# Kernel optimization log

Measured on AMD Instinct MI355X. Metric: run time of the kernel, lower is better.

## Reference

```python
import jax, jax.numpy as jnp
import numpy as np

THRESHOLD = 6.2
N_SECTIONS = 9      # n_conv_sections
SEC_LEN = 4         # n_section_length
SEC_H = 9           # n_input_sections + n_section_length - 1
BATCH = 16384


def setup_inputs() -> dict:
    key = jax.random.key(0)
    k1, k2 = jax.random.split(key)
    # input spike-wave tensor [T, C=1, H=41, W=40]
    x = jax.random.uniform(k1, (BATCH, 1, 41, 40), dtype=jnp.float32)
    # per-section conv weights, N(0.8, 0.05) as in snn.Convolution init
    W = 0.8 + 0.05 * jax.random.normal(k2, (N_SECTIONS, 50, 1, 6, 40), dtype=jnp.float32)
    return {"x": x, "W": W}


def _conv(sec, w):
    # sec: [B,1,9,40], w: [50,1,6,40] -> [B,50,4,1]
    return jax.lax.conv_general_dilated(
        sec, w, window_strides=(1, 1), padding='VALID',
        dimension_numbers=('NCHW', 'OIHW', 'NCHW'))


def reference(x, W):
    # slice the 9 overlapping input sections -> [9, B, 1, 9, 40]
    sec = jnp.stack([x[:, :, i * SEC_LEN:i * SEC_LEN + SEC_H, :]
                     for i in range(N_SECTIONS)])
    pots = jax.vmap(_conv)(sec, W)                      # [9, B, 50, 4, 1]
    pots = jnp.max(pots, axis=3, keepdims=True)         # Pooling((4,1)) -> [9, B, 50, 1, 1]
    spks = jnp.where(pots > THRESHOLD, 1.0, 0.0).astype(pots.dtype)
    # concat sections along height (dim=2 of [B,C,H,W])
    pots_cat = jnp.moveaxis(pots[:, :, :, 0, :], 0, 2)  # [B, 50, 9, 1]
    spks_cat = jnp.moveaxis(spks[:, :, :, 0, :], 0, 2)  # [B, 50, 9, 1]
    return pots_cat, spks_cat
```

## Files before the change

### kernel.cpp

```cpp
#include <hip/hip_runtime.h>
#include <cstdint>
#include <cstddef>

#define NBATCH   16384
#define NSEC     9
#define NOC      50
#define NOCP     64
#define KPAD     256
#define KREAL    240
#define XROW     1640
#define XUNITS   208
#define XSF      1664
#define TB       16
#define OUTHALF  7372800
#define THRESH   6.2f

typedef _Float16 half8  __attribute__((ext_vector_type(8)));
typedef float    f32x4  __attribute__((ext_vector_type(4)));

__global__ __launch_bounds__(256)
void wconv_kernel(const float* __restrict__ W, _Float16* __restrict__ wks) {
    int idx = blockIdx.x * 256 + threadIdx.x;
    int k   = idx & 255;
    int ocp = (idx >> 8) & 63;
    int sec = idx >> 14;
    float v = 0.0f;
    if (ocp < NOC && k < KREAL)
        v = W[(size_t)(sec * NOC + ocp) * KREAL + k];
    wks[idx] = (_Float16)v;
}

__global__ __launch_bounds__(256, 3)
void fused_kernel(const float* __restrict__ x,
                  const _Float16* __restrict__ wks,
                  float* __restrict__ out) {
    __shared__ __align__(16) _Float16 xs[TB * XSF];

    const int tid = threadIdx.x;
    const size_t b0 = (size_t)blockIdx.x * TB;

    {
        const int bb  = tid >> 4;
        const int u16 = tid & 15;
        const int sw  = bb & 7;
        const float* xrow = x + (b0 + bb) * XROW;
        _Float16* lrow = xs + bb * XSF;

        #pragma unroll
        for (int c = 0; c < 2; ++c) {
            const int jn = c ? 6 : 7;
            float4 va[7], vb[7];
            #pragma unroll
            for (int jj = 0; jj < 7; ++jj) {
                if (jj < jn) {
                    int u = u16 + 16 * (c * 7 + jj);
                    if (u < 205) {
                        va[jj] = *(const float4*)(xrow + u * 8);
                        vb[jj] = *(const float4*)(xrow + u * 8 + 4);
                    } else {
                        va[jj] = float4{0, 0, 0, 0};
                        vb[jj] = float4{0, 0, 0, 0};
                    }
                }
            }
            #pragma unroll
            for (int jj = 0; jj < 7; ++jj) {
                if (jj < jn) {
                    int u = u16 + 16 * (c * 7 + jj);
                    half8 h;
                    h[0] = (_Float16)va[jj].x; h[1] = (_Float16)va[jj].y;
                    h[2] = (_Float16)va[jj].z; h[3] = (_Float16)va[jj].w;
                    h[4] = (_Float16)vb[jj].x; h[5] = (_Float16)vb[jj].y;
                    h[6] = (_Float16)vb[jj].z; h[7] = (_Float16)vb[jj].w;
                    *(half8*)(lrow + ((u ^ sw) << 3)) = h;
                }
            }
        }
    }
    __syncthreads();

    const int lane = tid & 63;
    const int w    = tid >> 6;
    const int l15  = lane & 15;
    const int quad = lane >> 4;
    const int sw   = l15 & 7;

    const _Float16* arow = xs + l15 * XSF;
    const _Float16* wrow = wks + (size_t)(w * 16 + l15) * KPAD + quad * 8;

    f32x4 res[NSEC];

    for (int s = 0; s < NSEC; ++s) {
        const _Float16* wsec = wrow + (size_t)s * (NOCP * KPAD);
        half8 bv[8];
        #pragma unroll
        for (int kk = 0; kk < 8; ++kk)
            bv[kk] = *(const half8*)(wsec + kk * 32);

        f32x4 acc[4] = {f32x4{}, f32x4{}, f32x4{}, f32x4{}};
        const int su = s * 20 + quad;
        #pragma unroll
        for (int kk = 0; kk < 8; ++kk) {
            #pragma unroll
            for (int h = 0; h < 4; ++h) {
                int unit = su + h * 5 + kk * 4;
                half8 av = *(const half8*)(arow + ((unit ^ sw) << 3));
                acc[h] = __builtin_amdgcn_mfma_f32_16x16x32_f16(
                             av, bv[kk], acc[h], 0, 0, 0);
            }
        }
        f32x4 r;
        #pragma unroll
        for (int j = 0; j < 4; ++j)
            r[j] = fmaxf(fmaxf(acc[0][j], acc[1][j]),
                         fmaxf(acc[2][j], acc[3][j]));
        res[s] = r;
    }

    __syncthreads();
    float* t = (float*)xs;
    const int oc = w * 16 + l15;
    if (oc < NOC) {
        #pragma unroll
        for (int s = 0; s < NSEC; ++s)
            #pragma unroll
            for (int r = 0; r < 4; ++r)
                t[(quad * 4 + r) * 450 + oc * 9 + s] = res[s][r];
    }
    __syncthreads();

    const size_t ob = b0 * 450;
    for (int i = tid; i < TB * 450; i += 256) {
        float v = t[i];
        out[ob + i] = v;
        out[OUTHALF + ob + i] = (v > THRESH) ? 1.0f : 0.0f;
    }
}

__global__ __launch_bounds__(256)
void naive_kernel(const float* __restrict__ x, const float* __restrict__ W,
                  float* __restrict__ out) {
    size_t idx = (size_t)blockIdx.x * 256 + threadIdx.x;
    if (idx >= OUTHALF) return;
    int s  = (int)(idx % NSEC);
    int oc = (int)((idx / NSEC) % NOC);
    int b  = (int)(idx / (NSEC * NOC));
    const float* xb = x + (size_t)b * XROW + s * 160;
    const float* wv = W + (size_t)(s * NOC + oc) * KREAL;
    float best = -1e30f;
    for (int h0 = 0; h0 < 4; ++h0) {
        float acc = 0.0f;
        for (int k = 0; k < KREAL; ++k)
            acc += xb[h0 * 40 + k] * wv[k];
        best = fmaxf(best, acc);
    }
    out[idx] = best;
    out[OUTHALF + idx] = (best > THRESH) ? 1.0f : 0.0f;
}

extern "C" void kernel_launch(void* const* d_in, const int* in_sizes, int n_in,
                              void* d_out, int out_size, void* d_ws, size_t ws_size,
                              hipStream_t stream) {
    const float* x = (const float*)d_in[0];
    const float* W = (const float*)d_in[1];
    float* out = (float*)d_out;

    const size_t w_bytes = (size_t)NSEC * NOCP * KPAD * sizeof(_Float16);

    if (ws_size < w_bytes) {
        naive_kernel<<<(OUTHALF + 255) / 256, 256, 0, stream>>>(x, W, out);
        return;
    }

    _Float16* wks = (_Float16*)d_ws;

    wconv_kernel<<<(NSEC * NOCP * KPAD) / 256, 256, 0, stream>>>(W, wks);
    fused_kernel<<<NBATCH / TB, 256, 0, stream>>>(x, wks, out);
}
```

Baseline: 216.1 us.

## Pre-convert input to swizzled fp16 and DMA it into LDS, split sections across waves

A prep kernel now converts x to fp16 in a pre-swizzled tile layout alongside the weight conversion. The main kernel loads each tile straight into LDS with global_load_lds. Each wave now owns a subset of sections and computes all 64 output channels, reusing A fragments across four B tiles. This adds a full extra read/write pass over x in fp16 through workspace, and pooled potentials are rounded to fp16 before storing, which can flip threshold decisions near 6.2.

Measured after the change: 244.2 us. 13.0% more time.

```diff
diff --git a/kernel.cpp b/kernel.cpp
--- a/kernel.cpp
+++ b/kernel.cpp
@@ -12,95 +12,200 @@
 #define XUNITS   208
 #define XSF      1664
 #define TB       16
+#define NTILES   1024
+#define TILEF16  26624
+#define WELEMS   147456
+#define WBLOCKS  576
 #define OUTHALF  7372800
 #define THRESH   6.2f
 
 typedef _Float16 half8  __attribute__((ext_vector_type(8)));
+typedef _Float16 half4v __attribute__((ext_vector_type(4)));
 typedef float    f32x4  __attribute__((ext_vector_type(4)));
 
+#define GLD_LDS16(gsrc, ldst)                                                  \
+    __builtin_amdgcn_global_load_lds(                                          \
+        (const __attribute__((address_space(1))) void*)(gsrc),                 \
+        (__attribute__((address_space(3))) void*)(ldst), 16, 0, 0)
+
 __global__ __launch_bounds__(256)
-void wconv_kernel(const float* __restrict__ W, _Float16* __restrict__ wks) {
-    int idx = blockIdx.x * 256 + threadIdx.x;
-    int k   = idx & 255;
-    int ocp = (idx >> 8) & 63;
-    int sec = idx >> 14;
-    float v = 0.0f;
-    if (ocp < NOC && k < KREAL)
-        v = W[(size_t)(sec * NOC + ocp) * KREAL + k];
-    wks[idx] = (_Float16)v;
+void prep_kernel(const float* __restrict__ x, const float* __restrict__ W,
+                 _Float16* __restrict__ wks, _Float16* __restrict__ x16) {
+    const int blk = blockIdx.x, tid = threadIdx.x;
+    if (blk < WBLOCKS) {
+        int idx = blk * 256 + tid;
+        int k   = idx & 255;
+        int ocp = (idx >> 8) & 63;
+        int sec = idx >> 14;
+        float v = 0.0f;
+        if (ocp < NOC && k < KREAL)
+            v = W[(size_t)(sec * NOC + ocp) * KREAL + k];
+        wks[idx] = (_Float16)v;
+        return;
+    }
+    const int b2   = blk - WBLOCKS;
+    const int tile = b2 / 13;
+    const int rem  = (b2 - tile * 13) * 256 + tid;
+    const int brow = rem / XUNITS;
+    const int slot = rem - brow * XUNITS;
+    const int u    = slot ^ (brow & 7);
+    half8 h = {};
+    if (u < 205) {
+        const float* src = x + ((size_t)tile * TB + brow) * XROW + u * 8;
+        float4 a = *(const float4*)src;
+        float4 b = *(const float4*)(src + 4);
+        h[0] = (_Float16)a.x; h[1] = (_Float16)a.y;
+        h[2] = (_Float16)a.z; h[3] = (_Float16)a.w;
+        h[4] = (_Float16)b.x; h[5] = (_Float16)b.y;
+        h[6] = (_Float16)b.z; h[7] = (_Float16)b.w;
+    }
+    *(half8*)(x16 + (size_t)tile * TILEF16 + (size_t)rem * 8) = h;
 }
 
 __global__ __launch_bounds__(256, 3)
-void fused_kernel(const float* __restrict__ x,
-                  const _Float16* __restrict__ wks,
-                  float* __restrict__ out) {
+void fused_dma_kernel(const _Float16* __restrict__ x16,
+                      const _Float16* __restrict__ wks,
+                      float* __restrict__ out) {
     __shared__ __align__(16) _Float16 xs[TB * XSF];
 
+    const int tid  = threadIdx.x;
+    const int lane = tid & 63;
+    const int w    = tid >> 6;
+    const size_t b0 = (size_t)blockIdx.x * TB;
+
+    {
+        const _Float16* xt = x16 + (size_t)blockIdx.x * TILEF16;
+        #pragma unroll
+        for (int i = 0; i < 13; ++i) {
+            const int c = w * 13 + i;
+            GLD_LDS16(xt + c * 512 + lane * 8, xs + c * 512);
+        }
+    }
+    __syncthreads();
+
+    const int l15  = lane & 15;
+    const int quad = lane >> 4;
+    const int sw   = l15 & 7;
+
+    const _Float16* arow = xs + l15 * XSF;
+    const int s0 = (w == 0) ? 0 : (2 * w + 1);
+    const int ns = (w == 0) ? 3 : 2;
+
+    half4v res16[3][4];
+
+    #pragma unroll
+    for (int si = 0; si < 3; ++si) {
+        if (si < ns) {
+            const int s = s0 + si;
+            const _Float16* wsec = wks + ((size_t)s * NOCP + l15) * KPAD + quad * 8;
+            const int su = s * 20 + quad;
+            f32x4 acc[4][4] = {};
+            #pragma unroll
+            for (int kk = 0; kk < 8; ++kk) {
+                half8 av[4], bv[4];
+                #pragma unroll
+                for (int h = 0; h < 4; ++h) {
+                    int unit = su + h * 5 + kk * 4;
+                    av[h] = *(const half8*)(arow + ((unit ^ sw) << 3));
+                }
+                #pragma unroll
+                for (int n = 0; n < 4; ++n)
+                    bv[n] = *(const half8*)(wsec + n * 16 * KPAD + kk * 32);
+                #pragma unroll
+                for (int h = 0; h < 4; ++h)
+                    #pragma unroll
+                    for (int n = 0; n < 4; ++n)
+                        acc[h][n] = __builtin_amdgcn_mfma_f32_16x16x32_f16(
+                                        av[h], bv[n], acc[h][n], 0, 0, 0);
+            }
+            #pragma unroll
+            for (int n = 0; n < 4; ++n) {
+                half4v r;
+                #pragma unroll
+                for (int j = 0; j < 4; ++j)
+                    r[j] = (_Float16)fmaxf(
+                               fmaxf(acc[0][n][j], acc[1][n][j]),
+                               fmaxf(acc[2][n][j], acc[3][n][j]));
+                res16[si][n] = r;
+            }
+        }
+    }
+
+    __syncthreads();
+    float* t = (float*)xs;
+    #pragma unroll
+    for (int si = 0; si < 3; ++si) {
+        if (si < ns) {
+            const int s = s0 + si;
+            #pragma unroll
+            for (int n = 0; n < 4; ++n) {
+                const int oc = n * 16 + l15;
+                if (oc < NOC) {
+                    #pragma unroll
+                    for (int j = 0; j < 4; ++j)
+                        t[(quad * 4 + j) * 450 + oc * 9 + s] =
+                            (float)res16[si][n][j];
+                }
+            }
+        }
+    }
+    __syncthreads();
+
+    const size_t ob = b0 * 450;
+    for (int i = tid; i < TB * 450; i += 256) {
+        float v = t[i];
+        out[ob + i] = v;
+        out[OUTHALF + ob + i] = (v > THRESH) ? 1.0f : 0.0f;
+    }
+}
+
+__global__ __launch_bounds__(256, 3)
+void fused_reg_kernel(const float* __restrict__ x,
+                      const _Float16* __restrict__ wks,
+                      float* __restrict__ out) {
+    __shared__ __align__(16) _Float16 xs[TB * XSF];
     const int tid = threadIdx.x;
     const size_t b0 = (size_t)blockIdx.x * TB;
-
     {
         const int bb  = tid >> 4;
         const int u16 = tid & 15;
-        const int sw  = bb & 7;
+        const int swb = bb & 7;
         const float* xrow = x + (b0 + bb) * XROW;
         _Float16* lrow = xs + bb * XSF;
-
-        #pragma unroll
-        for (int c = 0; c < 2; ++c) {
-            const int jn = c ? 6 : 7;
-            float4 va[7], vb[7];
-            #pragma unroll
-            for (int jj = 0; jj < 7; ++jj) {
-                if (jj < jn) {
-                    int u = u16 + 16 * (c * 7 + jj);
-                    if (u < 205) {
-                        va[jj] = *(const float4*)(xrow + u * 8);
-                        vb[jj] = *(const float4*)(xrow + u * 8 + 4);
-                    } else {
-                        va[jj] = float4{0, 0, 0, 0};
-                        vb[jj] = float4{0, 0, 0, 0};
-                    }
-                }
-            }
-            #pragma unroll
-            for (int jj = 0; jj < 7; ++jj) {
-                if (jj < jn) {
-                    int u = u16 + 16 * (c * 7 + jj);
-                    half8 h;
-                    h[0] = (_Float16)va[jj].x; h[1] = (_Float16)va[jj].y;
-                    h[2] = (_Float16)va[jj].z; h[3] = (_Float16)va[jj].w;
-                    h[4] = (_Float16)vb[jj].x; h[5] = (_Float16)vb[jj].y;
-                    h[6] = (_Float16)vb[jj].z; h[7] = (_Float16)vb[jj].w;
-                    *(half8*)(lrow + ((u ^ sw) << 3)) = h;
-                }
-            }
-        }
-    }
-    __syncthreads();
-
+        #pragma unroll
+        for (int jj = 0; jj < 13; ++jj) {
+            int u = u16 + 16 * jj;
+            half8 h = {};
+            if (u < 205) {
+                float4 va = *(const float4*)(xrow + u * 8);
+                float4 vb = *(const float4*)(xrow + u * 8 + 4);
+                h[0] = (_Float16)va.x; h[1] = (_Float16)va.y;
+                h[2] = (_Float16)va.z; h[3] = (_Float16)va.w;
+                h[4] = (_Float16)vb.x; h[5] = (_Float16)vb.y;
+                h[6] = (_Float16)vb.z; h[7] = (_Float16)vb.w;
+            }
+            *(half8*)(lrow + ((u ^ swb) << 3)) = h;
+        }
+    }
+    __syncthreads();
     const int lane = tid & 63;
     const int w    = tid >> 6;
     const int l15  = lane & 15;
     const int quad = lane >> 4;
     const int sw   = l15 & 7;
-
     const _Float16* arow = xs + l15 * XSF;
     const _Float16* wrow = wks + (size_t)(w * 16 + l15) * KPAD + quad * 8;
-
     f32x4 res[NSEC];
-
     for (int s = 0; s < NSEC; ++s) {
         const _Float16* wsec = wrow + (size_t)s * (NOCP * KPAD);
         half8 bv[8];
         #pragma unroll
         for (int kk = 0; kk < 8; ++kk)
             bv[kk] = *(const half8*)(wsec + kk * 32);
-
         f32x4 acc[4] = {f32x4{}, f32x4{}, f32x4{}, f32x4{}};
         const int su = s * 20 + quad;
         #pragma unroll
-        for (int kk = 0; kk < 8; ++kk) {
+        for (int kk = 0; kk < 8; ++kk)
             #pragma unroll
             for (int h = 0; h < 4; ++h) {
                 int unit = su + h * 5 + kk * 4;
@@ -108,7 +213,6 @@
                 acc[h] = __builtin_amdgcn_mfma_f32_16x16x32_f16(
                              av, bv[kk], acc[h], 0, 0, 0);
             }
-        }
         f32x4 r;
         #pragma unroll
         for (int j = 0; j < 4; ++j)
@@ -116,7 +220,6 @@
                          fmaxf(acc[2][j], acc[3][j]));
         res[s] = r;
     }
-
     __syncthreads();
     float* t = (float*)xs;
     const int oc = w * 16 + l15;
@@ -128,7 +231,6 @@
                 t[(quad * 4 + r) * 450 + oc * 9 + s] = res[s][r];
     }
     __syncthreads();
-
     const size_t ob = b0 * 450;
     for (int i = tid; i < TB * 450; i += 256) {
         float v = t[i];
@@ -165,15 +267,19 @@
     const float* W = (const float*)d_in[1];
     float* out = (float*)d_out;
 
-    const size_t w_bytes = (size_t)NSEC * NOCP * KPAD * sizeof(_Float16);
-
-    if (ws_size < w_bytes) {
+    const size_t w_bytes   = (size_t)WELEMS * sizeof(_Float16);
+    const size_t x16_bytes = (size_t)NTILES * TILEF16 * sizeof(_Float16);
+
+    if (ws_size >= w_bytes + x16_bytes) {
+        _Float16* wks = (_Float16*)d_ws;
+        _Float16* x16 = (_Float16*)((char*)d_ws + w_bytes);
+        prep_kernel<<<WBLOCKS + NTILES * 13, 256, 0, stream>>>(x, W, wks, x16);
+        fused_dma_kernel<<<NTILES, 256, 0, stream>>>(x16, wks, out);
+    } else if (ws_size >= w_bytes) {
+        _Float16* wks = (_Float16*)d_ws;
+        prep_kernel<<<WBLOCKS, 256, 0, stream>>>(x, W, wks, nullptr);
+        fused_reg_kernel<<<NBATCH / TB, 256, 0, stream>>>(x, wks, out);
+    } else {
         naive_kernel<<<(OUTHALF + 255) / 256, 256, 0, stream>>>(x, W, out);
-        return;
-    }
-
-    _Float16* wks = (_Float16*)d_ws;
-
-    wconv_kernel<<<(NSEC * NOCP * KPAD) / 256, 256, 0, stream>>>(W, wks);
-    fused_kernel<<<NBATCH / TB, 256, 0, stream>>>(x, wks, out);
-}
+    }
+}
```
